# Optimization experiments

Hardware: AMD Instinct MI355X
Metric: run time of the kernel (lower is better)

## Reference

```python
import jax, jax.numpy as jnp
import numpy as np

WIN = 7
K1, K2 = 0.01, 0.03
NP_ = WIN ** 3
COV_NORM = NP_ / (NP_ - 1)


def _box3d(x, win=WIN):
    # Separable box filter: three 1D VALID convs (same math as the dense
    for ax in range(3):
        kshape = [1, 1, 1, 1, 1]
        kshape[2 + ax] = win
        k = jnp.ones(kshape, x.dtype) / win
        x = jax.lax.conv_general_dilated(
            x, k, window_strides=(1, 1, 1), padding='VALID',
            dimension_numbers=('NCDHW', 'OIDHW', 'NCDHW'))
    return x


def setup_inputs() -> dict:
    key = jax.random.key(0)
    k1, k2 = jax.random.split(key)
    B, C, D, H, W = 4, 1, 128, 128, 128
    X = jax.random.normal(k1, (B, C, D, H, W), dtype=jnp.float32)
    Y = jax.random.normal(k2, (B, C, D, H, W), dtype=jnp.float32)
    data_range = jnp.ones((B, 1, 1, 1, 1), dtype=jnp.float32)
    return {"X": X, "Y": Y, "data_range": data_range}


def reference(X, Y, data_range):
    C1 = (K1 * data_range) ** 2
    C2 = (K2 * data_range) ** 2
    ux = _box3d(X)
    uy = _box3d(Y)
    uxx = _box3d(X * X)
    uyy = _box3d(Y * Y)
    uxy = _box3d(X * Y)
    vx = COV_NORM * (uxx - ux * ux)
    vy = COV_NORM * (uyy - uy * uy)
    vxy = COV_NORM * (uxy - ux * uy)
    A1 = 2 * ux * uy + C1
    A2 = 2 * vxy + C2
    B1 = ux ** 2 + uy ** 2 + C1
    B2 = vx + vy + C2
    S = (A1 * A2) / (B1 * B2)
    return S.mean()
```

## Files before the change

kernel.cpp:

```cpp
#include <hip/hip_runtime.h>

#define NFULL 128
#define NOUT  122

#define S1_R 34
#define S1_Q 748
#define S1_B 3740
#define NBLK 1024

__device__ __forceinline__ void phaseA_task(const float* __restrict__ px,
                                            const float* __restrict__ py,
                                            float* __restrict__ s1p)
{
    float xs[8], ys[8];
#pragma unroll
    for (int k = 0; k < 4; ++k) {
        float2 tx = *(const float2*)(px + 2 * k);
        float2 ty = *(const float2*)(py + 2 * k);
        xs[2 * k] = tx.x; xs[2 * k + 1] = tx.y;
        ys[2 * k] = ty.x; ys[2 * k + 1] = ty.y;
    }
    float sx = 0.f, sy = 0.f, sxx = 0.f, syy = 0.f, sxy = 0.f;
#pragma unroll
    for (int k = 0; k < 7; ++k) {
        sx += xs[k]; sy += ys[k];
        sxx = fmaf(xs[k], xs[k], sxx);
        syy = fmaf(ys[k], ys[k], syy);
        sxy = fmaf(xs[k], ys[k], sxy);
    }
    float tx2 = sx - xs[0] + xs[7];
    float ty2 = sy - ys[0] + ys[7];
    float txx = sxx - xs[0] * xs[0] + xs[7] * xs[7];
    float tyy = syy - ys[0] * ys[0] + ys[7] * ys[7];
    float txy = sxy - xs[0] * ys[0] + xs[7] * ys[7];
    *(float2*)(s1p + 0 * S1_Q) = make_float2(sx,  tx2);
    *(float2*)(s1p + 1 * S1_Q) = make_float2(sy,  ty2);
    *(float2*)(s1p + 2 * S1_Q) = make_float2(sxx, txx);
    *(float2*)(s1p + 3 * S1_Q) = make_float2(syy, tyy);
    *(float2*)(s1p + 4 * S1_Q) = make_float2(sxy, txy);
}

__global__ __launch_bounds__(256, 4)
void ssim3d_kernel(const float* __restrict__ X, const float* __restrict__ Y,
                   const float* __restrict__ DR, double* __restrict__ ws, int mode)
{
    __shared__ __align__(16) float s1[2 * S1_B];

    const int tid = threadIdx.x;
    int bi = blockIdx.x;
    const int bb = bi & 3;  bi >>= 2;
    const int ht = bi & 7;  bi >>= 3;
    const int wt = bi & 3;  bi >>= 2;
    const int dc = bi;

    const int h0 = ht << 4;
    const int w0 = (wt == 3) ? 90 : (wt << 5);
    const int w_hi = (wt == 3) ? 122 : ((wt == 2) ? 90 : (w0 + 32));
    const int csize = (dc < 2) ? 16 : 15;
    const int d0 = (dc < 2) ? (dc << 4) : (32 + (dc - 2) * 15);
    const int nsl = csize + 6;

    const float dr = DR[bb];
    const float c1s = (0.01f * dr) * (0.01f * dr) * 117649.0f;
    const float c2s = (0.03f * dr) * (0.03f * dr) * 117649.0f;
    const float tni = 1.0f / 343.0f;
    const float kkA = 2.0f * 117649.0f / 342.0f;
    const float kkB = 117649.0f / 342.0f;

    const int sA  = tid & 15;
    const int rA0 = tid >> 4;
    const int rA1 = 16 + (tid >> 4);
    int grA0 = h0 + rA0; if (grA0 > NFULL - 1) grA0 = NFULL - 1;
    int grA1 = h0 + rA1; if (grA1 > NFULL - 1) grA1 = NFULL - 1;
    const int coffA = w0 + 2 * sA;

    const int sC = tid & 15, hC = tid >> 4;
    const int gh  = h0 + hC;
    const int gw0 = w0 + 2 * sC;
    const bool vh = (gh < NOUT);
    const bool vld0 = vh && (gw0 < w_hi);
    const bool vld1 = vh && (gw0 + 1 < w_hi);

    const size_t planeStride = (size_t)NFULL * NFULL;
    const size_t bbase = (size_t)bb * NFULL * planeStride;

    float2 ring[7][5];
    float2 run[5];
#pragma unroll
    for (int k = 0; k < 7; ++k)
#pragma unroll
        for (int q = 0; q < 5; ++q) ring[k][q] = make_float2(0.f, 0.f);
#pragma unroll
    for (int q = 0; q < 5; ++q) run[q] = make_float2(0.f, 0.f);
    float acc = 0.0f;

    for (int base = 0; base <= nsl; base += 7) {
#pragma unroll
        for (int u = 0; u < 7; ++u) {
            const int s = base + u;
            if (s <= nsl) {
                if (s < nsl) {
                    float* dst = s1 + (size_t)((s & 1) * S1_B);
                    const int dIn = d0 + s;
                    const float* Xp = X + bbase + (size_t)dIn * planeStride;
                    const float* Yp = Y + bbase + (size_t)dIn * planeStride;
                    phaseA_task(Xp + grA0 * NFULL + coffA, Yp + grA0 * NFULL + coffA,
                                dst + rA0 * S1_R + 2 * sA);
                    if (tid < 96)
                        phaseA_task(Xp + grA1 * NFULL + coffA, Yp + grA1 * NFULL + coffA,
                                    dst + rA1 * S1_R + 2 * sA);
                }
                if (s >= 1) {
                    const float* src = s1 + (size_t)(((s - 1) & 1) * S1_B)
                                          + hC * S1_R + 2 * sC;
                    const int slot = (u + 6) % 7;
#pragma unroll
                    for (int q = 0; q < 5; ++q) {
                        const float* p = src + q * S1_Q;
                        float2 h = *(const float2*)p;
#pragma unroll
                        for (int r = 1; r < 7; ++r) {
                            float2 v = *(const float2*)(p + r * S1_R);
                            h.x += v.x; h.y += v.y;
                        }
                        run[q].x += h.x - ring[slot][q].x;
                        run[q].y += h.y - ring[slot][q].y;
                        ring[slot][q] = h;
                    }
                    if (s >= 7) {
#pragma unroll
                        for (int j = 0; j < 2; ++j) {
                            const bool vld = j ? vld1 : vld0;
                            if (vld) {
                                float Sx  = j ? run[0].y : run[0].x;
                                float Sy  = j ? run[1].y : run[1].x;
                                float Sxx = j ? run[2].y : run[2].x;
                                float Syy = j ? run[3].y : run[3].x;
                                float Sxy = j ? run[4].y : run[4].x;
                                float P = Sx * Sy;
                                float Q = fmaf(Sx, Sx, Sy * Sy);
                                float A1 = fmaf(2.f, P, c1s);
                                float A2 = fmaf(kkA, fmaf(-tni, P, Sxy), c2s);
                                float B1 = Q + c1s;
                                float B2 = fmaf(kkB, fmaf(-tni, Q, Sxx + Syy), c2s);
                                float num = A1 * A2;
                                float den = B1 * B2;
                                float r0 = __builtin_amdgcn_rcpf(den);
                                r0 = r0 * fmaf(-den, r0, 2.0f);
                                acc = fmaf(num, r0, acc);
                            }
                        }
                    }
                }
                __syncthreads();
            }
        }
    }

#pragma unroll
    for (int off = 32; off; off >>= 1) acc += __shfl_down(acc, off);
    if ((tid & 63) == 0) s1[tid >> 6] = acc;
    __syncthreads();
    if (tid == 0) {
        double t = (double)s1[0] + (double)s1[1] + (double)s1[2] + (double)s1[3];
        if (mode) ws[blockIdx.x] = t;
        else      atomicAdd(ws, t);
    }
}

__global__ void ssim3d_finalize(const double* __restrict__ ws, float* __restrict__ out, int mode)
{
    if (mode) {
        __shared__ double sm[4];
        const int tid = threadIdx.x;
        double t = 0.0;
        for (int i = tid; i < NBLK; i += 256) t += ws[i];
#pragma unroll
        for (int off = 32; off; off >>= 1) t += __shfl_down(t, off);
        if ((tid & 63) == 0) sm[tid >> 6] = t;
        __syncthreads();
        if (tid == 0) {
            double r = sm[0] + sm[1] + sm[2] + sm[3];
            out[0] = (float)(r * (1.0 / 7263392.0));
        }
    } else {
        if (threadIdx.x == 0)
            out[0] = (float)(ws[0] * (1.0 / 7263392.0));
    }
}

extern "C" void kernel_launch(void* const* d_in, const int* in_sizes, int n_in,
                              void* d_out, int out_size, void* d_ws, size_t ws_size,
                              hipStream_t stream)
{
    const float* X  = (const float*)d_in[0];
    const float* Y  = (const float*)d_in[1];
    const float* DR = (const float*)d_in[2];
    double* ws = (double*)d_ws;

    const int mode = (ws_size >= NBLK * sizeof(double)) ? 1 : 0;
    if (!mode) hipMemsetAsync(d_ws, 0, sizeof(double), stream);
    ssim3d_kernel<<<NBLK, 256, 0, stream>>>(X, Y, DR, ws, mode);
    ssim3d_finalize<<<1, 256, 0, stream>>>(ws, (float*)d_out, mode);
}
```

Before: 123.0 us.

## Add separate H-pass with sliding window, enlarge depth chunks, fuse final reduction

The box filter along H becomes its own stage. 160 threads run a sliding-window sum over the W-filtered shared buffer into a second shared buffer, so each output thread no longer does seven loads per quantity. Depth chunks grow from 15-16 to 20-21 slices, which cuts the grid from 1024 to 768 blocks and lowers the 6-slice halo overhead per block. The separate finalize kernel is replaced by a last-block-done atomic counter reduction. In exchange the pipeline gains an extra stage, shared memory use rises (launch bounds drop to 3 blocks per CU), and 768 blocks may fill the CUs less evenly.

```diff
diff --git a/kernel.cpp b/kernel.cpp
--- a/kernel.cpp
+++ b/kernel.cpp
@@ -2,15 +2,18 @@
 
 #define NFULL 128
 #define NOUT  122
-
-#define S1_R 34
-#define S1_Q 748
-#define S1_B 3740
-#define NBLK 1024
+#define NBLK  768
+
+#define WROW 34
+#define WQ   748
+#define WB   3740
+#define HROW 34
+#define HQ   544
+#define HB   2720
 
 __device__ __forceinline__ void phaseA_task(const float* __restrict__ px,
                                             const float* __restrict__ py,
-                                            float* __restrict__ s1p)
+                                            float* __restrict__ wp)
 {
     float xs[8], ys[8];
 #pragma unroll
@@ -33,18 +36,23 @@
     float txx = sxx - xs[0] * xs[0] + xs[7] * xs[7];
     float tyy = syy - ys[0] * ys[0] + ys[7] * ys[7];
     float txy = sxy - xs[0] * ys[0] + xs[7] * ys[7];
-    *(float2*)(s1p + 0 * S1_Q) = make_float2(sx,  tx2);
-    *(float2*)(s1p + 1 * S1_Q) = make_float2(sy,  ty2);
-    *(float2*)(s1p + 2 * S1_Q) = make_float2(sxx, txx);
-    *(float2*)(s1p + 3 * S1_Q) = make_float2(syy, tyy);
-    *(float2*)(s1p + 4 * S1_Q) = make_float2(sxy, txy);
-}
-
-__global__ __launch_bounds__(256, 4)
+    *(float2*)(wp + 0 * WQ) = make_float2(sx,  tx2);
+    *(float2*)(wp + 1 * WQ) = make_float2(sy,  ty2);
+    *(float2*)(wp + 2 * WQ) = make_float2(sxx, txx);
+    *(float2*)(wp + 3 * WQ) = make_float2(syy, tyy);
+    *(float2*)(wp + 4 * WQ) = make_float2(sxy, txy);
+}
+
+__global__ __launch_bounds__(256, 3)
 void ssim3d_kernel(const float* __restrict__ X, const float* __restrict__ Y,
-                   const float* __restrict__ DR, double* __restrict__ ws, int mode)
-{
-    __shared__ __align__(16) float s1[2 * S1_B];
+                   const float* __restrict__ DR, double* __restrict__ ws,
+                   float* __restrict__ out, int mode)
+{
+    __shared__ __align__(16) float wbuf[2 * WB];
+    __shared__ __align__(16) float hbuf[2 * HB];
+    __shared__ float  redf[4];
+    __shared__ double redd[4];
+    __shared__ int lastFlag;
 
     const int tid = threadIdx.x;
     int bi = blockIdx.x;
@@ -56,8 +64,8 @@
     const int h0 = ht << 4;
     const int w0 = (wt == 3) ? 90 : (wt << 5);
     const int w_hi = (wt == 3) ? 122 : ((wt == 2) ? 90 : (w0 + 32));
-    const int csize = (dc < 2) ? 16 : 15;
-    const int d0 = (dc < 2) ? (dc << 4) : (32 + (dc - 2) * 15);
+    const int csize = (dc < 2) ? 21 : 20;
+    const int d0 = (dc < 2) ? dc * 21 : 42 + (dc - 2) * 20;
     const int nsl = csize + 6;
 
     const float dr = DR[bb];
@@ -69,10 +77,22 @@
 
     const int sA  = tid & 15;
     const int rA0 = tid >> 4;
-    const int rA1 = 16 + (tid >> 4);
     int grA0 = h0 + rA0; if (grA0 > NFULL - 1) grA0 = NFULL - 1;
-    int grA1 = h0 + rA1; if (grA1 > NFULL - 1) grA1 = NFULL - 1;
     const int coffA = w0 + 2 * sA;
+    const int eA = tid - 192;
+    int rA1 = 0, cA1 = 0, grA1 = 0, rA2 = 0, cA2 = 0, grA2 = 0;
+    if (eA >= 0) {
+        rA1 = 16 + (eA >> 4); cA1 = eA & 15;
+        grA1 = h0 + rA1; if (grA1 > NFULL - 1) grA1 = NFULL - 1;
+        if (eA < 32) {
+            const int t = eA + 64;
+            rA2 = 16 + (t >> 4); cA2 = t & 15;
+            grA2 = h0 + rA2; if (grA2 > NFULL - 1) grA2 = NFULL - 1;
+        }
+    }
+
+    const int bq = tid >> 5;
+    const int bc = tid & 31;
 
     const int sC = tid & 15, hC = tid >> 4;
     const int gh  = h0 + hC;
@@ -94,40 +114,52 @@
     for (int q = 0; q < 5; ++q) run[q] = make_float2(0.f, 0.f);
     float acc = 0.0f;
 
-    for (int base = 0; base <= nsl; base += 7) {
+    for (int base = 0; base <= nsl + 1; base += 7) {
 #pragma unroll
         for (int u = 0; u < 7; ++u) {
             const int s = base + u;
-            if (s <= nsl) {
+            if (s <= nsl + 1) {
                 if (s < nsl) {
-                    float* dst = s1 + (size_t)((s & 1) * S1_B);
+                    float* dst = wbuf + (size_t)((s & 1) * WB);
                     const int dIn = d0 + s;
                     const float* Xp = X + bbase + (size_t)dIn * planeStride;
                     const float* Yp = Y + bbase + (size_t)dIn * planeStride;
                     phaseA_task(Xp + grA0 * NFULL + coffA, Yp + grA0 * NFULL + coffA,
-                                dst + rA0 * S1_R + 2 * sA);
-                    if (tid < 96)
-                        phaseA_task(Xp + grA1 * NFULL + coffA, Yp + grA1 * NFULL + coffA,
-                                    dst + rA1 * S1_R + 2 * sA);
+                                dst + rA0 * WROW + 2 * sA);
+                    if (eA >= 0) {
+                        const int co1 = w0 + 2 * cA1;
+                        phaseA_task(Xp + grA1 * NFULL + co1, Yp + grA1 * NFULL + co1,
+                                    dst + rA1 * WROW + 2 * cA1);
+                        if (eA < 32) {
+                            const int co2 = w0 + 2 * cA2;
+                            phaseA_task(Xp + grA2 * NFULL + co2, Yp + grA2 * NFULL + co2,
+                                        dst + rA2 * WROW + 2 * cA2);
+                        }
+                    }
                 }
-                if (s >= 1) {
-                    const float* src = s1 + (size_t)(((s - 1) & 1) * S1_B)
-                                          + hC * S1_R + 2 * sC;
-                    const int slot = (u + 6) % 7;
+                if (s >= 1 && tid < 160) {
+                    const float* src = wbuf + (size_t)(((s - 1) & 1) * WB) + bq * WQ + bc;
+                    float* dst = hbuf + (size_t)(((s - 1) & 1) * HB) + bq * HQ + bc;
+                    float win = src[0] + src[WROW] + src[2 * WROW] + src[3 * WROW]
+                              + src[4 * WROW] + src[5 * WROW];
+#pragma unroll
+                    for (int h = 0; h < 16; ++h) {
+                        win += src[(h + 6) * WROW];
+                        dst[h * HROW] = win;
+                        win -= src[h * WROW];
+                    }
+                }
+                if (s >= 2) {
+                    const float* src = hbuf + (size_t)((s & 1) * HB) + hC * HROW + 2 * sC;
+                    const int slot = (u + 5) % 7;
 #pragma unroll
                     for (int q = 0; q < 5; ++q) {
-                        const float* p = src + q * S1_Q;
-                        float2 h = *(const float2*)p;
-#pragma unroll
-                        for (int r = 1; r < 7; ++r) {
-                            float2 v = *(const float2*)(p + r * S1_R);
-                            h.x += v.x; h.y += v.y;
-                        }
-                        run[q].x += h.x - ring[slot][q].x;
-                        run[q].y += h.y - ring[slot][q].y;
-                        ring[slot][q] = h;
-                    }
-                    if (s >= 7) {
+                        float2 h2 = *(const float2*)(src + q * HQ);
+                        run[q].x += h2.x - ring[slot][q].x;
+                        run[q].y += h2.y - ring[slot][q].y;
+                        ring[slot][q] = h2;
+                    }
+                    if (s >= 8) {
 #pragma unroll
                         for (int j = 0; j < 2; ++j) {
                             const bool vld = j ? vld1 : vld0;
@@ -159,34 +191,41 @@
 
 #pragma unroll
     for (int off = 32; off; off >>= 1) acc += __shfl_down(acc, off);
-    if ((tid & 63) == 0) s1[tid >> 6] = acc;
+    if ((tid & 63) == 0) redf[tid >> 6] = acc;
     __syncthreads();
-    if (tid == 0) {
-        double t = (double)s1[0] + (double)s1[1] + (double)s1[2] + (double)s1[3];
-        if (mode) ws[blockIdx.x] = t;
-        else      atomicAdd(ws, t);
-    }
-}
-
-__global__ void ssim3d_finalize(const double* __restrict__ ws, float* __restrict__ out, int mode)
-{
+
     if (mode) {
-        __shared__ double sm[4];
-        const int tid = threadIdx.x;
-        double t = 0.0;
-        for (int i = tid; i < NBLK; i += 256) t += ws[i];
-#pragma unroll
-        for (int off = 32; off; off >>= 1) t += __shfl_down(t, off);
-        if ((tid & 63) == 0) sm[tid >> 6] = t;
+        if (tid == 0) {
+            double t = (double)redf[0] + (double)redf[1] + (double)redf[2] + (double)redf[3];
+            ws[blockIdx.x] = t;
+            __threadfence();
+            unsigned int old = atomicAdd((unsigned int*)(ws + NBLK), 1u);
+            lastFlag = (old == NBLK - 1) ? 1 : 0;
+        }
         __syncthreads();
+        if (lastFlag) {
+            __threadfence();
+            double t = 0.0;
+            for (int i = tid; i < NBLK; i += 256) t += ws[i];
+#pragma unroll
+            for (int off = 32; off; off >>= 1) t += __shfl_down(t, off);
+            if ((tid & 63) == 0) redd[tid >> 6] = t;
+            __syncthreads();
+            if (tid == 0)
+                out[0] = (float)((redd[0] + redd[1] + redd[2] + redd[3])
+                                 * (1.0 / 7263392.0));
+        }
+    } else {
         if (tid == 0) {
-            double r = sm[0] + sm[1] + sm[2] + sm[3];
-            out[0] = (float)(r * (1.0 / 7263392.0));
-        }
-    } else {
-        if (threadIdx.x == 0)
-            out[0] = (float)(ws[0] * (1.0 / 7263392.0));
-    }
+            double t = (double)redf[0] + (double)redf[1] + (double)redf[2] + (double)redf[3];
+            atomicAdd(ws, t);
+        }
+    }
+}
+
+__global__ void ssim3d_finalize(const double* __restrict__ ws, float* __restrict__ out)
+{
+    out[0] = (float)(ws[0] * (1.0 / 7263392.0));
 }
 
 extern "C" void kernel_launch(void* const* d_in, const int* in_sizes, int n_in,
@@ -198,8 +237,12 @@
     const float* DR = (const float*)d_in[2];
     double* ws = (double*)d_ws;
 
-    const int mode = (ws_size >= NBLK * sizeof(double)) ? 1 : 0;
-    if (!mode) hipMemsetAsync(d_ws, 0, sizeof(double), stream);
-    ssim3d_kernel<<<NBLK, 256, 0, stream>>>(X, Y, DR, ws, mode);
-    ssim3d_finalize<<<1, 256, 0, stream>>>(ws, (float*)d_out, mode);
-}
+    const int mode = (ws_size >= (size_t)(NBLK + 1) * sizeof(double)) ? 1 : 0;
+    if (mode)
+        hipMemsetAsync((char*)d_ws + (size_t)NBLK * sizeof(double), 0, sizeof(double), stream);
+    else
+        hipMemsetAsync(d_ws, 0, sizeof(double), stream);
+
+    ssim3d_kernel<<<NBLK, 256, 0, stream>>>(X, Y, DR, ws, (float*)d_out, mode);
+    if (!mode) ssim3d_finalize<<<1, 1, 0, stream>>>(ws, (float*)d_out);
+}
```

Result: slower. 146.3 us (+18.9%).
